# Optimization experiments

Hardware: AMD Instinct MI355X
Metric: run time of the kernel (lower is better)

Reference implementation:

```python
import jax, jax.numpy as jnp
import numpy as np

N_NODES = 50000


def _sage_conv(x, src, dst, W_l, b_l, W_r, n_nodes):
    # mean-aggregate neighbor (source) features onto targets
    msg = x[src]                                   # [E, d_in] gather
    agg = jax.ops.segment_sum(msg, dst, num_segments=n_nodes)   # [N, d_in]
    deg = jax.ops.segment_sum(jnp.ones((src.shape[0],), x.dtype), dst,
                              num_segments=n_nodes)
    agg = agg / jnp.clip(deg, 1.0, None)[:, None]  # mean with deg>=1 clamp (PyG)
    # out = lin_l(agg) + lin_r(x)   (bias lives in lin_l)
    return agg @ W_l.T + b_l + x @ W_r.T


def setup_inputs() -> dict:
    key = jax.random.key(0)
    ks = jax.random.split(key, 8)
    d_in, d_hid, d_out = 128, 256, 128
    n_edges = 800000
    x = jax.random.normal(ks[0], (N_NODES, d_in), dtype=jnp.float32)
    edge_index = jax.random.randint(ks[1], (2, n_edges), 0, N_NODES, dtype=jnp.int32)
    def glorot(k, shape):
        lim = float(np.sqrt(6.0 / (shape[0] + shape[1])))
        return jax.random.uniform(k, shape, jnp.float32, -lim, lim)
    return {
        "x": x,
        "edge_index": edge_index,
        "W1l": glorot(ks[2], (d_hid, d_in)),
        "b1": jnp.zeros((d_hid,), jnp.float32),
        "W1r": glorot(ks[3], (d_hid, d_in)),
        "W2l": glorot(ks[4], (d_out, d_hid)),
        "b2": jnp.zeros((d_out,), jnp.float32),
        "W2r": glorot(ks[5], (d_out, d_hid)),
    }


def reference(x, edge_index, W1l, b1, W1r, W2l, b2, W2r):
    src, dst = edge_index[0], edge_index[1]
    h = jax.nn.relu(_sage_conv(x, src, dst, W1l, b1, W1r, N_NODES))
    out = _sage_conv(h, src, dst, W2l, b2, W2r, N_NODES)
    return out
```

## Files before the change

### kernel.cpp

```cpp
#include <hip/hip_runtime.h>
#include <hip/hip_bf16.h>

#define NN 50000
#define NN_PAD 50176
#define NE 800000
#define NB 196
#define CAP 6144
#define EPB 4096

typedef __attribute__((ext_vector_type(8))) short short8;
typedef __attribute__((ext_vector_type(4))) float f32x4;

__device__ __forceinline__ unsigned short f2bf(float f) {
    union { float f; unsigned u; } v; v.f = f;
    unsigned u = v.u;
    return (unsigned short)((u + 0x7fffu + ((u >> 16) & 1u)) >> 16);
}
__device__ __forceinline__ float bfu_lo(unsigned u) {
    union { unsigned u; float f; } v; v.u = u << 16; return v.f;
}
__device__ __forceinline__ float bfu_hi(unsigned u) {
    union { unsigned u; float f; } v; v.u = u & 0xffff0000u; return v.f;
}

__global__ void k_setup(const float* __restrict__ W1l, const float* __restrict__ W1r,
                        const float* __restrict__ W2l, const float* __restrict__ W2r,
                        unsigned short* __restrict__ W1pk, unsigned short* __restrict__ W2pk,
                        const float4* __restrict__ x4, unsigned short* __restrict__ x_bf,
                        int* __restrict__ gcursor) {
    int blk = blockIdx.x, t = threadIdx.x;
    if (blk < 64) {
        int tid = blk * 256 + t;
        int table = tid >> 13;
        int r = tid & 8191;
        int lane = r & 63, ni = (r >> 6) & 3, ks = (r >> 8) & 7, g = r >> 11;
        int lm = lane & 15, lq = lane >> 4;
        int o = g * 64 + ni * 16 + lm;
        int k = ks * 32 + lq * 8;
        unsigned short v[8];
        if (table == 0) {
            if (k < 128) {
#pragma unroll
                for (int j = 0; j < 8; ++j) v[j] = f2bf(W1l[o * 128 + k + j]);
            } else {
#pragma unroll
                for (int j = 0; j < 8; ++j) v[j] = f2bf(W1r[o * 128 + k - 128 + j]);
            }
            *(uint4*)(W1pk + (size_t)r * 8) = *(const uint4*)v;
        } else {
            if (o < 128) {
#pragma unroll
                for (int j = 0; j < 8; ++j) v[j] = f2bf(W2l[o * 256 + k + j]);
            } else {
#pragma unroll
                for (int j = 0; j < 8; ++j) v[j] = f2bf(W2r[(o - 128) * 256 + k + j]);
            }
            *(uint4*)(W2pk + (size_t)r * 8) = *(const uint4*)v;
        }
    } else if (blk < 6314) {
        int gid = (blk - 64) * 256 + t;
        int n = gid >> 5, c = gid & 31;
        float4 v = x4[(size_t)n * 32 + c];
        ushort4 o;
        o.x = f2bf(v.x); o.y = f2bf(v.y); o.z = f2bf(v.z); o.w = f2bf(v.w);
        *(ushort4*)(x_bf + (size_t)n * 128 + c * 4) = o;
    } else {
        gcursor[t] = t * CAP;
    }
}

__global__ void k_part(const int* __restrict__ src, const int* __restrict__ dst,
                       int* __restrict__ gcursor, unsigned* __restrict__ pairs) {
    __shared__ int cnt[256];
    __shared__ int base[256];
    int t = threadIdx.x;
    cnt[t] = 0;
    __syncthreads();
    int e0 = blockIdx.x * EPB;
    int eend = min(e0 + EPB, NE);
    int rank[16], bk[16];
    unsigned pk[16];
    int m = 0;
    for (int e = e0 + t; e < eend; e += 256) {
        int s = src[e], d = dst[e];
        bk[m] = d >> 8;
        pk[m] = ((unsigned)s << 8) | (unsigned)(d & 255);
        rank[m] = atomicAdd(&cnt[bk[m]], 1);
        ++m;
    }
    __syncthreads();
    if (t < NB && cnt[t] > 0) base[t] = atomicAdd(&gcursor[t], cnt[t]);
    __syncthreads();
    for (int i = 0; i < m; ++i) {
        int pos = base[bk[i]] + rank[i];
        if (pos < (bk[i] + 1) * CAP) pairs[pos] = pk[i];
    }
}

__global__ void k_build(const int* __restrict__ gcursor, const unsigned* __restrict__ pairs,
                        int* __restrict__ deg_i, int* __restrict__ row_start,
                        int* __restrict__ esrc) {
    __shared__ int buf[256];
    __shared__ int ldeg[256];
    __shared__ int lstart[256];
    __shared__ int sh_base, sh_cnt;
    __shared__ int lsrc[CAP];
    int b = blockIdx.x, t = threadIdx.x;
    int c = (t < NB) ? min(gcursor[t] - t * CAP, CAP) : 0;
    buf[t] = c;
    __syncthreads();
#pragma unroll
    for (int o = 1; o < 256; o <<= 1) {
        int add = (t >= o) ? buf[t - o] : 0;
        __syncthreads();
        buf[t] += add;
        __syncthreads();
    }
    if (t == b) { sh_cnt = c; sh_base = buf[b] - c; }
    ldeg[t] = 0;
    __syncthreads();
    int cnt = sh_cnt, base = sh_base;
    int rank[CAP / 256], msrc[CAP / 256], mloc[CAP / 256];
    int m = 0;
    for (int e = t; e < cnt; e += 256) {
        unsigned p = pairs[(size_t)b * CAP + e];
        msrc[m] = (int)(p >> 8); mloc[m] = (int)(p & 255u);
        rank[m] = atomicAdd(&ldeg[mloc[m]], 1);
        ++m;
    }
    __syncthreads();
    int v = ldeg[t];
    buf[t] = v;
    __syncthreads();
#pragma unroll
    for (int o = 1; o < 256; o <<= 1) {
        int add = (t >= o) ? buf[t - o] : 0;
        __syncthreads();
        buf[t] += add;
        __syncthreads();
    }
    lstart[t] = buf[t] - v;
    int node = b * 256 + t;
    if (node < NN) { deg_i[node] = v; row_start[node] = base + lstart[t]; }
    else           { deg_i[node] = 0; row_start[node] = 0; }
    __syncthreads();
    for (int i = 0; i < m; ++i) lsrc[lstart[mloc[i]] + rank[i]] = msrc[i];
    __syncthreads();
    for (int e = t; e < cnt; e += 256) esrc[base + e] = lsrc[e];
}

__global__ __launch_bounds__(256) void k_fused(
        const unsigned short* __restrict__ x_bf, const int* __restrict__ deg_i,
        const int* __restrict__ row_start, const int* __restrict__ esrc,
        const unsigned short* __restrict__ W1pk, const unsigned short* __restrict__ W2pk,
        const float* __restrict__ b1, const float* __restrict__ b2,
        unsigned short* __restrict__ y2l, float* __restrict__ out) {
    __shared__ unsigned short T[16384];
    int t = threadIdx.x;
    int blk = blockIdx.x;

    {
        int nl = t >> 2, q = t & 3;
        int n = blk * 64 + nl;
        int mi = nl >> 4, lm = nl & 15;
        float acc[32];
#pragma unroll
        for (int j = 0; j < 32; ++j) acc[j] = 0.f;
        int dg = 0;
        if (n < NN) {
            dg = deg_i[n];
            int st = row_start[n];
            const unsigned short* bp = x_bf + q * 32;
            int i = 0;
            for (; i + 2 <= dg; i += 2) {
                int s0 = esrc[st + i], s1 = esrc[st + i + 1];
                const uint4* p0 = (const uint4*)(bp + (size_t)s0 * 128);
                const uint4* p1 = (const uint4*)(bp + (size_t)s1 * 128);
#pragma unroll
                for (int u = 0; u < 4; ++u) {
                    uint4 a = p0[u], b = p1[u];
                    acc[u*8+0] += bfu_lo(a.x) + bfu_lo(b.x); acc[u*8+1] += bfu_hi(a.x) + bfu_hi(b.x);
                    acc[u*8+2] += bfu_lo(a.y) + bfu_lo(b.y); acc[u*8+3] += bfu_hi(a.y) + bfu_hi(b.y);
                    acc[u*8+4] += bfu_lo(a.z) + bfu_lo(b.z); acc[u*8+5] += bfu_hi(a.z) + bfu_hi(b.z);
                    acc[u*8+6] += bfu_lo(a.w) + bfu_lo(b.w); acc[u*8+7] += bfu_hi(a.w) + bfu_hi(b.w);
                }
            }
            if (i < dg) {
                int s = esrc[st + i];
                const uint4* p0 = (const uint4*)(bp + (size_t)s * 128);
#pragma unroll
                for (int u = 0; u < 4; ++u) {
                    uint4 a = p0[u];
                    acc[u*8+0] += bfu_lo(a.x); acc[u*8+1] += bfu_hi(a.x);
                    acc[u*8+2] += bfu_lo(a.y); acc[u*8+3] += bfu_hi(a.y);
                    acc[u*8+4] += bfu_lo(a.z); acc[u*8+5] += bfu_hi(a.z);
                    acc[u*8+6] += bfu_lo(a.w); acc[u*8+7] += bfu_hi(a.w);
                }
            }
        }
        float invd = 1.0f / (float)max(dg, 1);
#pragma unroll
        for (int u = 0; u < 4; ++u) {
            unsigned short o[8];
#pragma unroll
            for (int j = 0; j < 8; ++j) o[j] = f2bf(acc[u*8+j] * invd);
            *(uint4*)(T + ((size_t)((q * 4 + mi) * 64 + lm + 16 * u)) * 8) = *(const uint4*)o;
        }
        if (n < NN) {
            const uint4* xs = (const uint4*)(x_bf + (size_t)n * 128 + q * 32);
#pragma unroll
            for (int u = 0; u < 4; ++u)
                *(uint4*)(T + ((size_t)(((4 + q) * 4 + mi) * 64 + lm + 16 * u)) * 8) = xs[u];
        } else {
            uint4 z = {0u, 0u, 0u, 0u};
#pragma unroll
            for (int u = 0; u < 4; ++u)
                *(uint4*)(T + ((size_t)(((4 + q) * 4 + mi) * 64 + lm + 16 * u)) * 8) = z;
        }
    }
    __syncthreads();

    int wave = t >> 6, lane = t & 63;
    int lm = lane & 15, lq = lane >> 4;

    f32x4 acc1[4][4];
#pragma unroll
    for (int mi = 0; mi < 4; ++mi)
#pragma unroll
        for (int ni = 0; ni < 4; ++ni) acc1[mi][ni] = (f32x4){0.f, 0.f, 0.f, 0.f};
    {
        const unsigned short* wb = W1pk + (size_t)wave * 8 * 4 * 64 * 8;
#pragma unroll 2
        for (int ks = 0; ks < 8; ++ks) {
            short8 a[4], b[4];
#pragma unroll
            for (int mi = 0; mi < 4; ++mi)
                a[mi] = *(const short8*)(T + ((size_t)((ks * 4 + mi) * 64 + lane)) * 8);
#pragma unroll
            for (int ni = 0; ni < 4; ++ni)
                b[ni] = *(const short8*)(wb + ((size_t)((ks * 4 + ni) * 64 + lane)) * 8);
#pragma unroll
            for (int mi = 0; mi < 4; ++mi)
#pragma unroll
                for (int ni = 0; ni < 4; ++ni)
                    acc1[mi][ni] = __builtin_amdgcn_mfma_f32_16x16x32_bf16(a[mi], b[ni], acc1[mi][ni], 0, 0, 0);
        }
    }
    __syncthreads();

#pragma unroll
    for (int ni = 0; ni < 4; ++ni) {
        int col = wave * 64 + ni * 16 + lm;
        float bv = b1[col];
        int ks = col >> 5, k32 = col & 31;
        int la = (k32 >> 3), j = col & 7;
#pragma unroll
        for (int mi = 0; mi < 4; ++mi)
#pragma unroll
            for (int r = 0; r < 4; ++r) {
                float v = fmaxf(acc1[mi][ni][r] + bv, 0.0f);
                int mrow16 = lq * 4 + r;
                T[((size_t)((ks * 4 + mi) * 64 + mrow16 + 16 * la)) * 8 + j] = f2bf(v);
            }
    }
    __syncthreads();

    f32x4 acc2[4][4];
#pragma unroll
    for (int mi = 0; mi < 4; ++mi)
#pragma unroll
        for (int ni = 0; ni < 4; ++ni) acc2[mi][ni] = (f32x4){0.f, 0.f, 0.f, 0.f};
    {
        const unsigned short* wb = W2pk + (size_t)wave * 8 * 4 * 64 * 8;
#pragma unroll 2
        for (int ks = 0; ks < 8; ++ks) {
            short8 a[4], b[4];
#pragma unroll
            for (int mi = 0; mi < 4; ++mi)
                a[mi] = *(const short8*)(T + ((size_t)((ks * 4 + mi) * 64 + lane)) * 8);
#pragma unroll
            for (int ni = 0; ni < 4; ++ni)
                b[ni] = *(const short8*)(wb + ((size_t)((ks * 4 + ni) * 64 + lane)) * 8);
#pragma unroll
            for (int mi = 0; mi < 4; ++mi)
#pragma unroll
                for (int ni = 0; ni < 4; ++ni)
                    acc2[mi][ni] = __builtin_amdgcn_mfma_f32_16x16x32_bf16(a[mi], b[ni], acc2[mi][ni], 0, 0, 0);
        }
    }

    if (wave < 2) {
#pragma unroll
        for (int ni = 0; ni < 4; ++ni) {
            int col = wave * 64 + ni * 16 + lm;
#pragma unroll
            for (int mi = 0; mi < 4; ++mi)
#pragma unroll
                for (int r = 0; r < 4; ++r) {
                    int row = blk * 64 + mi * 16 + lq * 4 + r;
                    y2l[(size_t)row * 128 + col] = f2bf(acc2[mi][ni][r]);
                }
        }
    } else {
#pragma unroll
        for (int ni = 0; ni < 4; ++ni) {
            int col = (wave - 2) * 64 + ni * 16 + lm;
            float bv = b2[col];
#pragma unroll
            for (int mi = 0; mi < 4; ++mi)
#pragma unroll
                for (int r = 0; r < 4; ++r) {
                    int row = blk * 64 + mi * 16 + lq * 4 + r;
                    if (row < NN) out[(size_t)row * 128 + col] = acc2[mi][ni][r] + bv;
                }
        }
    }
}

__global__ void k_agg_out(const uint4* __restrict__ yl4, const int* __restrict__ deg_i,
                          const int* __restrict__ row_start, const int* __restrict__ esrc,
                          float* __restrict__ out) {
    int gid = blockIdx.x * blockDim.x + threadIdx.x;
    int n = gid >> 4, c = gid & 15;
    int dg = deg_i[n], st = row_start[n];
    float acc[8] = {0.f, 0.f, 0.f, 0.f, 0.f, 0.f, 0.f, 0.f};
    int i = 0;
    for (; i + 2 <= dg; i += 2) {
        int s0 = esrc[st + i], s1 = esrc[st + i + 1];
        uint4 h0 = yl4[(size_t)s0 * 16 + c];
        uint4 h1 = yl4[(size_t)s1 * 16 + c];
        acc[0] += bfu_lo(h0.x) + bfu_lo(h1.x); acc[1] += bfu_hi(h0.x) + bfu_hi(h1.x);
        acc[2] += bfu_lo(h0.y) + bfu_lo(h1.y); acc[3] += bfu_hi(h0.y) + bfu_hi(h1.y);
        acc[4] += bfu_lo(h0.z) + bfu_lo(h1.z); acc[5] += bfu_hi(h0.z) + bfu_hi(h1.z);
        acc[6] += bfu_lo(h0.w) + bfu_lo(h1.w); acc[7] += bfu_hi(h0.w) + bfu_hi(h1.w);
    }
    if (i < dg) {
        int s = esrc[st + i];
        uint4 hv = yl4[(size_t)s * 16 + c];
        acc[0] += bfu_lo(hv.x); acc[1] += bfu_hi(hv.x);
        acc[2] += bfu_lo(hv.y); acc[3] += bfu_hi(hv.y);
        acc[4] += bfu_lo(hv.z); acc[5] += bfu_hi(hv.z);
        acc[6] += bfu_lo(hv.w); acc[7] += bfu_hi(hv.w);
    }
    float invd = 1.0f / (float)max(dg, 1);
    float* op = out + (size_t)n * 128 + c * 8;
    float4 o0 = *(float4*)op, o1 = *(float4*)(op + 4);
    o0.x += acc[0] * invd; o0.y += acc[1] * invd; o0.z += acc[2] * invd; o0.w += acc[3] * invd;
    o1.x += acc[4] * invd; o1.y += acc[5] * invd; o1.z += acc[6] * invd; o1.w += acc[7] * invd;
    *(float4*)op = o0; *(float4*)(op + 4) = o1;
}

extern "C" void kernel_launch(void* const* d_in, const int* in_sizes, int n_in,
                              void* d_out, int out_size, void* d_ws, size_t ws_size,
                              hipStream_t stream) {
    const float* x   = (const float*)d_in[0];
    const int*   ei  = (const int*)d_in[1];
    const int*   src = ei;
    const int*   dst = ei + NE;
    const float* W1l = (const float*)d_in[2];
    const float* b1  = (const float*)d_in[3];
    const float* W1r = (const float*)d_in[4];
    const float* W2l = (const float*)d_in[5];
    const float* b2  = (const float*)d_in[6];
    const float* W2r = (const float*)d_in[7];
    float* out = (float*)d_out;

    char* ws = (char*)d_ws;
    int* deg_i            = (int*)(ws + 0);
    int* row_start        = (int*)(ws + 200704);
    int* gcursor          = (int*)(ws + 401408);
    int* esrc             = (int*)(ws + 409600);
    unsigned* pairs       = (unsigned*)(ws + 4194304);
    unsigned short* x_bf  = (unsigned short*)(ws + 9437184);
    unsigned short* y2l   = (unsigned short*)(ws + 23068672);
    unsigned short* W1pk  = (unsigned short*)(ws + 36700160);
    unsigned short* W2pk  = (unsigned short*)(ws + 36831232);

    k_setup<<<6315, 256, 0, stream>>>(W1l, W1r, W2l, W2r, W1pk, W2pk,
                                      (const float4*)x, x_bf, gcursor);
    k_part<<<(NE + EPB - 1) / EPB, 256, 0, stream>>>(src, dst, gcursor, pairs);
    k_build<<<NB, 256, 0, stream>>>(gcursor, pairs, deg_i, row_start, esrc);
    k_fused<<<NN_PAD / 64, 256, 0, stream>>>(x_bf, deg_i, row_start, esrc,
                                             W1pk, W2pk, b1, b2, y2l, out);
    k_agg_out<<<NN * 16 / 256, 256, 0, stream>>>((const uint4*)y2l, deg_i, row_start, esrc, out);
}
```

Before: 223.6 us.

## Split fused layer-1 aggregation out of GEMM kernel into a separate gather kernel

Layer-1 mean aggregation moves out of the fused MFMA kernel into its own kernel, k_agg1. There each node is handled by 16 threads with 8 accumulators each, instead of 4 threads with 32 accumulators each. The kernel writes the concatenated [mean-agg | x] bf16 rows to a global buffer. The GEMM kernel then loads its A operands straight from that buffer instead of staging them in LDS. The aim is more memory-level parallelism and occupancy for the latency-bound gather. The cost is an extra ~25 MB global write and read plus one more kernel launch.

```diff
diff --git a/kernel.cpp b/kernel.cpp
--- a/kernel.cpp
+++ b/kernel.cpp
@@ -149,79 +149,49 @@
     for (int e = t; e < cnt; e += 256) esrc[base + e] = lsrc[e];
 }
 
-__global__ __launch_bounds__(256) void k_fused(
-        const unsigned short* __restrict__ x_bf, const int* __restrict__ deg_i,
-        const int* __restrict__ row_start, const int* __restrict__ esrc,
+__global__ void k_agg1(const uint4* __restrict__ xb4, const int* __restrict__ deg_i,
+                       const int* __restrict__ row_start, const int* __restrict__ esrc,
+                       unsigned short* __restrict__ Abar1) {
+    int gid = blockIdx.x * blockDim.x + threadIdx.x;
+    int n = gid >> 4, c = gid & 15;
+    int dg = deg_i[n], st = row_start[n];
+    float acc[8] = {0.f, 0.f, 0.f, 0.f, 0.f, 0.f, 0.f, 0.f};
+    int i = 0;
+    for (; i + 2 <= dg; i += 2) {
+        int s0 = esrc[st + i], s1 = esrc[st + i + 1];
+        uint4 h0 = xb4[(size_t)s0 * 16 + c];
+        uint4 h1 = xb4[(size_t)s1 * 16 + c];
+        acc[0] += bfu_lo(h0.x) + bfu_lo(h1.x); acc[1] += bfu_hi(h0.x) + bfu_hi(h1.x);
+        acc[2] += bfu_lo(h0.y) + bfu_lo(h1.y); acc[3] += bfu_hi(h0.y) + bfu_hi(h1.y);
+        acc[4] += bfu_lo(h0.z) + bfu_lo(h1.z); acc[5] += bfu_hi(h0.z) + bfu_hi(h1.z);
+        acc[6] += bfu_lo(h0.w) + bfu_lo(h1.w); acc[7] += bfu_hi(h0.w) + bfu_hi(h1.w);
+    }
+    if (i < dg) {
+        int s = esrc[st + i];
+        uint4 hv = xb4[(size_t)s * 16 + c];
+        acc[0] += bfu_lo(hv.x); acc[1] += bfu_hi(hv.x);
+        acc[2] += bfu_lo(hv.y); acc[3] += bfu_hi(hv.y);
+        acc[4] += bfu_lo(hv.z); acc[5] += bfu_hi(hv.z);
+        acc[6] += bfu_lo(hv.w); acc[7] += bfu_hi(hv.w);
+    }
+    float invd = 1.0f / (float)max(dg, 1);
+    unsigned short o[8];
+#pragma unroll
+    for (int j = 0; j < 8; ++j) o[j] = f2bf(acc[j] * invd);
+    *(uint4*)(Abar1 + (size_t)n * 256 + c * 8) = *(const uint4*)o;
+    *(uint4*)(Abar1 + (size_t)n * 256 + 128 + c * 8) = xb4[(size_t)n * 16 + c];
+}
+
+__global__ __launch_bounds__(256) void k_gemm12(
+        const unsigned short* __restrict__ Abar1,
         const unsigned short* __restrict__ W1pk, const unsigned short* __restrict__ W2pk,
         const float* __restrict__ b1, const float* __restrict__ b2,
         unsigned short* __restrict__ y2l, float* __restrict__ out) {
     __shared__ unsigned short T[16384];
-    int t = threadIdx.x;
-    int blk = blockIdx.x;
-
-    {
-        int nl = t >> 2, q = t & 3;
-        int n = blk * 64 + nl;
-        int mi = nl >> 4, lm = nl & 15;
-        float acc[32];
-#pragma unroll
-        for (int j = 0; j < 32; ++j) acc[j] = 0.f;
-        int dg = 0;
-        if (n < NN) {
-            dg = deg_i[n];
-            int st = row_start[n];
-            const unsigned short* bp = x_bf + q * 32;
-            int i = 0;
-            for (; i + 2 <= dg; i += 2) {
-                int s0 = esrc[st + i], s1 = esrc[st + i + 1];
-                const uint4* p0 = (const uint4*)(bp + (size_t)s0 * 128);
-                const uint4* p1 = (const uint4*)(bp + (size_t)s1 * 128);
-#pragma unroll
-                for (int u = 0; u < 4; ++u) {
-                    uint4 a = p0[u], b = p1[u];
-                    acc[u*8+0] += bfu_lo(a.x) + bfu_lo(b.x); acc[u*8+1] += bfu_hi(a.x) + bfu_hi(b.x);
-                    acc[u*8+2] += bfu_lo(a.y) + bfu_lo(b.y); acc[u*8+3] += bfu_hi(a.y) + bfu_hi(b.y);
-                    acc[u*8+4] += bfu_lo(a.z) + bfu_lo(b.z); acc[u*8+5] += bfu_hi(a.z) + bfu_hi(b.z);
-                    acc[u*8+6] += bfu_lo(a.w) + bfu_lo(b.w); acc[u*8+7] += bfu_hi(a.w) + bfu_hi(b.w);
-                }
-            }
-            if (i < dg) {
-                int s = esrc[st + i];
-                const uint4* p0 = (const uint4*)(bp + (size_t)s * 128);
-#pragma unroll
-                for (int u = 0; u < 4; ++u) {
-                    uint4 a = p0[u];
-                    acc[u*8+0] += bfu_lo(a.x); acc[u*8+1] += bfu_hi(a.x);
-                    acc[u*8+2] += bfu_lo(a.y); acc[u*8+3] += bfu_hi(a.y);
-                    acc[u*8+4] += bfu_lo(a.z); acc[u*8+5] += bfu_hi(a.z);
-                    acc[u*8+6] += bfu_lo(a.w); acc[u*8+7] += bfu_hi(a.w);
-                }
-            }
-        }
-        float invd = 1.0f / (float)max(dg, 1);
-#pragma unroll
-        for (int u = 0; u < 4; ++u) {
-            unsigned short o[8];
-#pragma unroll
-            for (int j = 0; j < 8; ++j) o[j] = f2bf(acc[u*8+j] * invd);
-            *(uint4*)(T + ((size_t)((q * 4 + mi) * 64 + lm + 16 * u)) * 8) = *(const uint4*)o;
-        }
-        if (n < NN) {
-            const uint4* xs = (const uint4*)(x_bf + (size_t)n * 128 + q * 32);
-#pragma unroll
-            for (int u = 0; u < 4; ++u)
-                *(uint4*)(T + ((size_t)(((4 + q) * 4 + mi) * 64 + lm + 16 * u)) * 8) = xs[u];
-        } else {
-            uint4 z = {0u, 0u, 0u, 0u};
-#pragma unroll
-            for (int u = 0; u < 4; ++u)
-                *(uint4*)(T + ((size_t)(((4 + q) * 4 + mi) * 64 + lm + 16 * u)) * 8) = z;
-        }
-    }
-    __syncthreads();
-
+    int t = threadIdx.x, blk = blockIdx.x;
     int wave = t >> 6, lane = t & 63;
     int lm = lane & 15, lq = lane >> 4;
+    int m0 = blk * 64;
 
     f32x4 acc1[4][4];
 #pragma unroll
@@ -229,13 +199,14 @@
 #pragma unroll
         for (int ni = 0; ni < 4; ++ni) acc1[mi][ni] = (f32x4){0.f, 0.f, 0.f, 0.f};
     {
-        const unsigned short* wb = W1pk + (size_t)wave * 8 * 4 * 64 * 8;
+        const unsigned short* ap = Abar1 + (size_t)(m0 + lm) * 256 + lq * 8;
+        const unsigned short* wb = W1pk + (size_t)wave * 16384;
 #pragma unroll 2
         for (int ks = 0; ks < 8; ++ks) {
             short8 a[4], b[4];
 #pragma unroll
             for (int mi = 0; mi < 4; ++mi)
-                a[mi] = *(const short8*)(T + ((size_t)((ks * 4 + mi) * 64 + lane)) * 8);
+                a[mi] = *(const short8*)(ap + (size_t)(mi * 16) * 256 + ks * 32);
 #pragma unroll
             for (int ni = 0; ni < 4; ++ni)
                 b[ni] = *(const short8*)(wb + ((size_t)((ks * 4 + ni) * 64 + lane)) * 8);
@@ -246,14 +217,13 @@
                     acc1[mi][ni] = __builtin_amdgcn_mfma_f32_16x16x32_bf16(a[mi], b[ni], acc1[mi][ni], 0, 0, 0);
         }
     }
-    __syncthreads();
 
 #pragma unroll
     for (int ni = 0; ni < 4; ++ni) {
         int col = wave * 64 + ni * 16 + lm;
         float bv = b1[col];
-        int ks = col >> 5, k32 = col & 31;
-        int la = (k32 >> 3), j = col & 7;
+        int ks = col >> 5;
+        int la = (col & 31) >> 3, j = col & 7;
 #pragma unroll
         for (int mi = 0; mi < 4; ++mi)
 #pragma unroll
@@ -271,7 +241,7 @@
 #pragma unroll
         for (int ni = 0; ni < 4; ++ni) acc2[mi][ni] = (f32x4){0.f, 0.f, 0.f, 0.f};
     {
-        const unsigned short* wb = W2pk + (size_t)wave * 8 * 4 * 64 * 8;
+        const unsigned short* wb = W2pk + (size_t)wave * 16384;
 #pragma unroll 2
         for (int ks = 0; ks < 8; ++ks) {
             short8 a[4], b[4];
@@ -373,14 +343,15 @@
     unsigned* pairs       = (unsigned*)(ws + 4194304);
     unsigned short* x_bf  = (unsigned short*)(ws + 9437184);
     unsigned short* y2l   = (unsigned short*)(ws + 23068672);
-    unsigned short* W1pk  = (unsigned short*)(ws + 36700160);
-    unsigned short* W2pk  = (unsigned short*)(ws + 36831232);
+    unsigned short* Abar1 = (unsigned short*)(ws + 36700160);
+    unsigned short* W1pk  = (unsigned short*)(ws + 62914560);
+    unsigned short* W2pk  = (unsigned short*)(ws + 63045632);
 
     k_setup<<<6315, 256, 0, stream>>>(W1l, W1r, W2l, W2r, W1pk, W2pk,
                                       (const float4*)x, x_bf, gcursor);
     k_part<<<(NE + EPB - 1) / EPB, 256, 0, stream>>>(src, dst, gcursor, pairs);
     k_build<<<NB, 256, 0, stream>>>(gcursor, pairs, deg_i, row_start, esrc);
-    k_fused<<<NN_PAD / 64, 256, 0, stream>>>(x_bf, deg_i, row_start, esrc,
-                                             W1pk, W2pk, b1, b2, y2l, out);
+    k_agg1<<<NN * 16 / 256, 256, 0, stream>>>((const uint4*)x_bf, deg_i, row_start, esrc, Abar1);
+    k_gemm12<<<NN_PAD / 64, 256, 0, stream>>>(Abar1, W1pk, W2pk, b1, b2, y2l, out);
     k_agg_out<<<NN * 16 / 256, 256, 0, stream>>>((const uint4*)y2l, deg_i, row_start, esrc, out);
 }
```

After: 229.9 us. 1.03x slower.
